# Kernel tuning notes

Measured on AMD Instinct MI355X. Metric: run time of the kernel, lower is better.

The kernel has to match this reference:

```python
import jax, jax.numpy as jnp
import numpy as np

B, S, DIM, FF = 64, 577, 768, 3072
BLK = 8          # block_shape = (8, 8)
DENSITY = 0.1    # fraction of 8x8 blocks that are nonzero


def _expand_block_mask(m):
    # m: [out//BLK, in//BLK] bool -> [out, in] float mask
    return jnp.repeat(jnp.repeat(m, BLK, axis=0), BLK, axis=1)


def setup_inputs() -> dict:
    key = jax.random.key(0)
    ks = jax.random.split(key, 7)
    x = jax.random.normal(ks[0], (B, S, DIM), dtype=jnp.float32)
    # nn.Linear-style init scale
    W1 = jax.random.normal(ks[1], (FF, DIM), dtype=jnp.float32) / np.sqrt(DIM).astype(np.float32)
    b1 = jax.random.normal(ks[2], (FF,), dtype=jnp.float32) * 0.02
    W2 = jax.random.normal(ks[3], (DIM, FF), dtype=jnp.float32) / np.sqrt(FF).astype(np.float32)
    b2 = jax.random.normal(ks[4], (DIM,), dtype=jnp.float32) * 0.02
    mask1 = jax.random.uniform(ks[5], (FF // BLK, DIM // BLK)) < DENSITY
    mask2 = jax.random.uniform(ks[6], (DIM // BLK, FF // BLK)) < DENSITY
    return {"x": x, "W1": W1, "b1": b1, "W2": W2, "b2": b2,
            "mask1": mask1, "mask2": mask2}


def reference(x, W1, b1, W2, b2, mask1, mask2):
    # fc1: block-sparse linear  y = x @ (W1 * M1)^T + b1
    Wm1 = W1 * _expand_block_mask(mask1).astype(W1.dtype)  # [FF, DIM]
    h = jnp.einsum('bsd,fd->bsf', x, Wm1) + b1             # [B, S, FF]
    h = jax.nn.gelu(h, approximate=False)                  # F.gelu default (exact)
    # fc2: block-sparse linear
    Wm2 = W2 * _expand_block_mask(mask2).astype(W2.dtype)  # [DIM, FF]
    return jnp.einsum('bsf,df->bsd', h, Wm2) + b2          # [B, S, DIM]
```

## Files before the change

### kernel.cpp

```cpp
#include <hip/hip_runtime.h>
#include <hip/hip_bf16.h>


typedef __attribute__((ext_vector_type(8))) short short8;
typedef __attribute__((ext_vector_type(4))) float f32x4;
typedef unsigned long long u64;
typedef unsigned short ushort_t;

#define DIM 768
#define FF 3072
#define NF16 192
#define ND16 48
#define NDB 96
#define NFB 384
#define MR 16
#define XP 776
#define HP 1544

#define S1CAP (NF16 * 96)
#define S2CAP (ND16 * 2 * 192)
#define W1S_TOT (S1CAP * 128)
#define W2S_TOT (S2CAP * 128)

__device__ __forceinline__ float gelu_fast(float v) {
    float t = v * fmaf(v * v, 0.07135548f, 1.5957691f);
    return v / (1.0f + __expf(-t));
}
__device__ __forceinline__ ushort_t f2bs(float f) {
    union { __hip_bfloat16 h; ushort_t u; } cv;
    cv.h = __float2bfloat16(f);
    return cv.u;
}

__global__ __launch_bounds__(64)
void prep_count(const int* __restrict__ mask1, const int* __restrict__ mask2,
                int* __restrict__ off1, int* __restrict__ off2)
{
    const int l = threadIdx.x;
    const int g = blockIdx.x;
    if (g < NF16) {
        const int* r0 = mask1 + (2 * g) * NDB;
        const int* r1 = r0 + NDB;
        bool ua = (r0[l] | r1[l]) != 0;
        u64 ba = __ballot(ua);
        bool ub = (l < 32) && ((r0[64 + l] | r1[64 + l]) != 0);
        u64 bb = __ballot(ub);
        if (l == 0) {
            int cnt = __popcll(ba) + __popcll(bb);
            off1[g + 1] = (cnt + 7) & ~7;
        }
    } else {
        const int G = g - NF16;
        const int* r0 = mask2 + (2 * G) * NFB;
        const int* r1 = r0 + NFB;
        int c0 = 0, c1 = 0;
        #pragma unroll
        for (int p = 0; p < 6; ++p) {
            u64 b = __ballot((r0[p * 64 + l] | r1[p * 64 + l]) != 0);
            if (p < 3) c0 += __popcll(b); else c1 += __popcll(b);
        }
        if (l == 0) {
            off2[0 * ND16 + G + 1] = (c0 + 7) & ~7;
            off2[1 * ND16 + G + 1] = (c1 + 7) & ~7;
        }
    }
}

__global__ __launch_bounds__(64)
void prep_scan(int* __restrict__ off1, int* __restrict__ off2)
{
    if (threadIdx.x == 0) {
        off1[0] = 0;
        for (int i = 0; i < NF16; ++i) off1[i + 1] += off1[i];
    } else if (threadIdx.x == 1) {
        off2[0] = 0;
        for (int i = 0; i < 2 * ND16; ++i) off2[i + 1] += off2[i];
    }
}

__global__ __launch_bounds__(256)
void prep_gather(const float* __restrict__ W1, const float* __restrict__ W2,
                 const int* __restrict__ mask1, const int* __restrict__ mask2,
                 const int* __restrict__ off1, const int* __restrict__ off2,
                 __hip_bfloat16* __restrict__ w1s, __hip_bfloat16* __restrict__ w2s,
                 ushort_t* __restrict__ idx1s, ushort_t* __restrict__ idx2s)
{
    __shared__ ushort_t sidx[192];
    __shared__ int sc[1];
    const int tid = threadIdx.x;
    const int l = tid & 63;
    const int g = blockIdx.x;

    if (g < NF16) {
        const int F = g;
        const int* r0 = mask1 + (2 * F) * NDB;
        const int* r1 = r0 + NDB;
        if (tid < 64) {
            bool ua = (r0[l] | r1[l]) != 0;
            u64 ba = __ballot(ua);
            bool ub = (l < 32) && ((r0[64 + l] | r1[64 + l]) != 0);
            u64 bb = __ballot(ub);
            int ca = __popcll(ba);
            if (ua) sidx[__popcll(ba & ((1ull << l) - 1ull))] = (ushort_t)l;
            if (ub) sidx[ca + __popcll(bb & ((1ull << l) - 1ull))] = (ushort_t)(64 + l);
            int cnt = ca + __popcll(bb);
            if (l == 0) {
                sc[0] = cnt;
                int cntp = (cnt + 7) & ~7;
                for (int i = cnt; i < cntp; ++i) sidx[i] = 0;
            }
        }
        __syncthreads();
        const int cnt = sc[0];
        const int base = off1[F];
        const int cntp = off1[F + 1] - base;
        if (tid < cntp) idx1s[base + tid] = sidx[tid];
        for (int e = tid; e < cntp * 128; e += 256) {
            int slot = e >> 7, r = (e >> 3) & 15, j = e & 7;
            int db = sidx[slot];
            float w = 0.f;
            if (slot < cnt && mask1[(2 * F + (r >> 3)) * NDB + db])
                w = W1[(long)(F * 16 + r) * DIM + db * 8 + j];
            w1s[(long)base * 128 + e] = __float2bfloat16(w);
        }
    } else {
        const int gi = g - NF16;
        const int c = gi / ND16;
        const int G = gi % ND16;
        const int* r0 = mask2 + (2 * G) * NFB;
        const int* r1 = r0 + NFB;
        if (tid < 64) {
            u64 b[3]; int pc[3];
            #pragma unroll
            for (int p = 0; p < 3; ++p) {
                int fb = c * 192 + p * 64 + l;
                b[p] = __ballot((r0[fb] | r1[fb]) != 0);
                pc[p] = __popcll(b[p]);
            }
            int basea = 0;
            #pragma unroll
            for (int p = 0; p < 3; ++p) {
                if ((b[p] >> l) & 1ull)
                    sidx[basea + __popcll(b[p] & ((1ull << l) - 1ull))] = (ushort_t)(p * 64 + l);
                basea += pc[p];
            }
            if (l == 0) {
                int cnt = basea;
                sc[0] = cnt;
                int cntp = (cnt + 7) & ~7;
                for (int i = cnt; i < cntp; ++i) sidx[i] = 0;
            }
        }
        __syncthreads();
        const int cnt = sc[0];
        const int base = off2[c * ND16 + G];
        const int cntp = off2[c * ND16 + G + 1] - base;
        if (tid < cntp) idx2s[base + tid] = sidx[tid];
        for (int e = tid; e < cntp * 128; e += 256) {
            int slot = e >> 7, r = (e >> 3) & 15, j = e & 7;
            int lfb = sidx[slot];
            int fb = c * 192 + lfb;
            float w = 0.f;
            if (slot < cnt && mask2[(2 * G + (r >> 3)) * NFB + fb])
                w = W2[(long)(G * 16 + r) * FF + fb * 8 + j];
            w2s[(long)base * 128 + e] = __float2bfloat16(w);
        }
    }
}

#define PREF(IDXS, WS, ARR, ROWOFF)                                          \
    {                                                                        \
        int sp = (s < sEnd) ? s : sEnd - 8;                                  \
        uint4 q = *(const uint4*)(IDXS + sp);                                \
        unsigned dd0 = (lg & 2) ? q.y : q.x;                                 \
        unsigned dd1 = (lg & 2) ? q.w : q.z;                                 \
        int m0 = (int)((dd0 >> shsel) & 0xffffu);                            \
        int m1 = (int)((dd1 >> shsel) & 0xffffu);                            \
        pa0 = *(const short8*)&ARR[ROWOFF + m0 * 8];                         \
        pa1 = *(const short8*)&ARR[ROWOFF + m1 * 8];                         \
        const ushort_t* wp = WS + (long)sp * 128 + lofs;                     \
        pw0 = *(const short8*)(wp);                                          \
        pw1 = *(const short8*)(wp + 512);                                    \
    }

#define STEP(IDXS, WS, ARR, ROWOFF)                                          \
    {                                                                        \
        short8 a0 = pa0, a1 = pa1, w0 = pw0, w1 = pw1;                       \
        s += 8;                                                              \
        PREF(IDXS, WS, ARR, ROWOFF)                                          \
        ca = __builtin_amdgcn_mfma_f32_16x16x32_bf16(a0, w0, ca, 0, 0, 0);   \
        cb = __builtin_amdgcn_mfma_f32_16x16x32_bf16(a1, w1, cb, 0, 0, 0);   \
    }

__global__ __launch_bounds__(512, 4)
void bsffn_main(const float* __restrict__ x,
                const float* __restrict__ pb1, const float* __restrict__ pb2,
                const ushort_t* __restrict__ w1s, const ushort_t* __restrict__ w2s,
                const ushort_t* __restrict__ idx1s, const ushort_t* __restrict__ idx2s,
                const int* __restrict__ off1, const int* __restrict__ off2,
                float* __restrict__ out)
{
    __shared__ __align__(16) ushort_t xs[MR * XP];
    __shared__ __align__(16) ushort_t hs[MR * HP];

    const int tid = threadIdx.x;
    const int wave = tid >> 6;
    const int l = tid & 63;
    const int l15 = l & 15;
    const int lg = l >> 4;
    const int xrow = l15 * XP;
    const int hrow = l15 * HP;
    const int lofs = lg * 128 + l15 * 8;
    const unsigned shsel = (unsigned)((lg & 1) << 4);
    const long rowBase = (long)blockIdx.x * MR;

    {
        const float* xr = x + rowBase * DIM;
        #pragma unroll
        for (int i = 0; i < 3; ++i) {
            int e = tid + i * 512;
            int row = e / 96, c8 = e % 96;
            const float4 v0 = *(const float4*)(xr + row * DIM + c8 * 8);
            const float4 v1 = *(const float4*)(xr + row * DIM + c8 * 8 + 4);
            uint4 wv;
            wv.x = (unsigned)f2bs(v0.x) | ((unsigned)f2bs(v0.y) << 16);
            wv.y = (unsigned)f2bs(v0.z) | ((unsigned)f2bs(v0.w) << 16);
            wv.z = (unsigned)f2bs(v1.x) | ((unsigned)f2bs(v1.y) << 16);
            wv.w = (unsigned)f2bs(v1.z) | ((unsigned)f2bs(v1.w) << 16);
            *(uint4*)&xs[row * XP + c8 * 8] = wv;
        }
    }

    f32x4 acc[6];
    #pragma unroll
    for (int t = 0; t < 6; ++t) acc[t] = (f32x4){0.f, 0.f, 0.f, 0.f};

    __syncthreads();

    for (int chunk = 0; chunk < 2; ++chunk) {
        {
            const int Fbeg = chunk * 96 + wave * 12;
            int s = off1[Fbeg];
            const int sEnd = off1[Fbeg + 12];
            short8 pa0 = {0,0,0,0,0,0,0,0}, pa1 = pa0, pw0 = pa0, pw1 = pa0;
            if (s < sEnd) PREF(idx1s, w1s, xs, xrow)
            #pragma unroll 1
            for (int j = 0; j < 12; ++j) {
                const int F = Fbeg + j;
                const int gend = off1[F + 1];
                const float bias = pb1[F * 16 + l15];
                f32x4 ca = {0.f,0.f,0.f,0.f}, cb = {0.f,0.f,0.f,0.f};
                while (s < gend) STEP(idx1s, w1s, xs, xrow)
                const int Fl = F - chunk * 96;
                #pragma unroll
                for (int r = 0; r < 4; ++r) {
                    float v = gelu_fast(ca[r] + cb[r] + bias);
                    hs[(lg * 4 + r) * HP + Fl * 16 + l15] = f2bs(v);
                }
            }
        }
        __syncthreads();

        {
            const int Pbeg = chunk * ND16 + wave * 6;
            int s = off2[Pbeg];
            const int sEnd = off2[Pbeg + 6];
            short8 pa0 = {0,0,0,0,0,0,0,0}, pa1 = pa0, pw0 = pa0, pw1 = pa0;
            if (s < sEnd) PREF(idx2s, w2s, hs, hrow)
#define FC2G(J)                                                              \
            {                                                                \
                const int gend = off2[Pbeg + (J) + 1];                       \
                f32x4 ca = acc[J], cb = {0.f,0.f,0.f,0.f};                   \
                while (s < gend) STEP(idx2s, w2s, hs, hrow)                  \
                acc[J] = ca + cb;                                            \
            }
            FC2G(0) FC2G(1) FC2G(2) FC2G(3) FC2G(4) FC2G(5)
#undef FC2G
        }
        __syncthreads();
    }

    float* sacc = (float*)hs;
    #pragma unroll
    for (int j = 0; j < 6; ++j) {
        const int d = (wave * 6 + j) * 16 + l15;
        #pragma unroll
        for (int r = 0; r < 4; ++r)
            sacc[(lg * 4 + r) * 772 + d] = acc[j][r];
    }
    __syncthreads();
    {
        const float4* pb24 = (const float4*)pb2;
        #pragma unroll
        for (int i = 0; i < 6; ++i) {
            int e = tid + i * 512;
            int row = e / 192, c4 = e % 192;
            float4 v = *(const float4*)&sacc[row * 772 + c4 * 4];
            float4 b = pb24[c4];
            v.x += b.x; v.y += b.y; v.z += b.z; v.w += b.w;
            *(float4*)&out[(rowBase + row) * DIM + c4 * 4] = v;
        }
    }
}

extern "C" void kernel_launch(void* const* d_in, const int* in_sizes, int n_in,
                              void* d_out, int out_size, void* d_ws, size_t ws_size,
                              hipStream_t stream) {
    const float* x = (const float*)d_in[0];
    const float* W1 = (const float*)d_in[1];
    const float* b1 = (const float*)d_in[2];
    const float* W2 = (const float*)d_in[3];
    const float* b2 = (const float*)d_in[4];
    const int* mask1 = (const int*)d_in[5];
    const int* mask2 = (const int*)d_in[6];
    float* out = (float*)d_out;

    ushort_t* w1s = (ushort_t*)d_ws;
    ushort_t* w2s = w1s + W1S_TOT;
    ushort_t* idx1s = w2s + W2S_TOT;
    ushort_t* idx2s = idx1s + S1CAP;
    int* off1 = (int*)(idx2s + S2CAP);
    int* off2 = off1 + (NF16 + 1);

    prep_count<<<NF16 + ND16, 64, 0, stream>>>(mask1, mask2, off1, off2);
    prep_scan<<<1, 64, 0, stream>>>(off1, off2);
    prep_gather<<<NF16 + 2 * ND16, 256, 0, stream>>>(
        W1, W2, mask1, mask2, off1, off2,
        (__hip_bfloat16*)w1s, (__hip_bfloat16*)w2s, idx1s, idx2s);

    const int rows = in_sizes[0] / DIM;
    const int nblk = rows / MR;
    bsffn_main<<<nblk, 512, 0, stream>>>(
        x, b1, b2, w1s, w2s, idx1s, idx2s, off1, off2, out);
}
```

Measured before the change: 340.7 us.

## Process 32 rows per block to reuse sparse weight fragments across two MFMA row tiles

Doubles the rows per workgroup from 16 to 32 so each loaded sparse weight fragment feeds two MFMA row tiles, halving weight traffic per output row. The slot loop is restructured into double-buffered pair steps of 16 slots, so group padding goes from 8 to 16 and the buffers get extra capacity. GELU is rewritten to use exp2f with prefolded constants. The cost is more registers and shared memory per block, so launch bounds drop to 2 blocks per CU, and the larger padding adds wasted zero MFMAs.

Measured after the change: 335.8 us. About the same (-1.4%).

```diff
diff --git a/kernel.cpp b/kernel.cpp
--- a/kernel.cpp
+++ b/kernel.cpp
@@ -13,18 +13,22 @@
 #define ND16 48
 #define NDB 96
 #define NFB 384
-#define MR 16
+#define MR 32
 #define XP 776
 #define HP 1544
-
-#define S1CAP (NF16 * 96)
-#define S2CAP (ND16 * 2 * 192)
+#define XSEC (16 * XP)
+#define HSEC (16 * HP)
+
+#define S1CAP (NF16 * 96 + 32)
+#define S2CAP (ND16 * 2 * 192 + 32)
 #define W1S_TOT (S1CAP * 128)
 #define W2S_TOT (S2CAP * 128)
 
+#define MFMA __builtin_amdgcn_mfma_f32_16x16x32_bf16
+
 __device__ __forceinline__ float gelu_fast(float v) {
-    float t = v * fmaf(v * v, 0.07135548f, 1.5957691f);
-    return v / (1.0f + __expf(-t));
+    float t2 = v * fmaf(v * v, -0.10295667f, -2.30235629f);
+    return v / (1.0f + exp2f(t2));
 }
 __device__ __forceinline__ ushort_t f2bs(float f) {
     union { __hip_bfloat16 h; ushort_t u; } cv;
@@ -47,7 +51,7 @@
         u64 bb = __ballot(ub);
         if (l == 0) {
             int cnt = __popcll(ba) + __popcll(bb);
-            off1[g + 1] = (cnt + 7) & ~7;
+            off1[g + 1] = (cnt + 15) & ~15;
         }
     } else {
         const int G = g - NF16;
@@ -60,8 +64,8 @@
             if (p < 3) c0 += __popcll(b); else c1 += __popcll(b);
         }
         if (l == 0) {
-            off2[0 * ND16 + G + 1] = (c0 + 7) & ~7;
-            off2[1 * ND16 + G + 1] = (c1 + 7) & ~7;
+            off2[0 * ND16 + G + 1] = (c0 + 15) & ~15;
+            off2[1 * ND16 + G + 1] = (c1 + 15) & ~15;
         }
     }
 }
@@ -106,8 +110,8 @@
             int cnt = ca + __popcll(bb);
             if (l == 0) {
                 sc[0] = cnt;
-                int cntp = (cnt + 7) & ~7;
-                for (int i = cnt; i < cntp; ++i) sidx[i] = 0;
+                int cntp = (cnt + 15) & ~15;
+                for (int i = cnt; i < cntp && i < 192; ++i) sidx[i] = 0;
             }
         }
         __syncthreads();
@@ -147,8 +151,8 @@
             if (l == 0) {
                 int cnt = basea;
                 sc[0] = cnt;
-                int cntp = (cnt + 7) & ~7;
-                for (int i = cnt; i < cntp; ++i) sidx[i] = 0;
+                int cntp = (cnt + 15) & ~15;
+                for (int i = cnt; i < cntp && i < 192; ++i) sidx[i] = 0;
             }
         }
         __syncthreads();
@@ -168,31 +172,37 @@
     }
 }
 
-#define PREF(IDXS, WS, ARR, ROWOFF)                                          \
-    {                                                                        \
-        int sp = (s < sEnd) ? s : sEnd - 8;                                  \
-        uint4 q = *(const uint4*)(IDXS + sp);                                \
-        unsigned dd0 = (lg & 2) ? q.y : q.x;                                 \
-        unsigned dd1 = (lg & 2) ? q.w : q.z;                                 \
-        int m0 = (int)((dd0 >> shsel) & 0xffffu);                            \
-        int m1 = (int)((dd1 >> shsel) & 0xffffu);                            \
-        pa0 = *(const short8*)&ARR[ROWOFF + m0 * 8];                         \
-        pa1 = *(const short8*)&ARR[ROWOFF + m1 * 8];                         \
-        const ushort_t* wp = WS + (long)sp * 128 + lofs;                     \
-        pw0 = *(const short8*)(wp);                                          \
-        pw1 = *(const short8*)(wp + 512);                                    \
-    }
-
-#define STEP(IDXS, WS, ARR, ROWOFF)                                          \
-    {                                                                        \
-        short8 a0 = pa0, a1 = pa1, w0 = pw0, w1 = pw1;                       \
-        s += 8;                                                              \
-        PREF(IDXS, WS, ARR, ROWOFF)                                          \
-        ca = __builtin_amdgcn_mfma_f32_16x16x32_bf16(a0, w0, ca, 0, 0, 0);   \
-        cb = __builtin_amdgcn_mfma_f32_16x16x32_bf16(a1, w1, cb, 0, 0, 0);   \
-    }
-
-__global__ __launch_bounds__(512, 4)
+#define PREF(BUF, IP, WP, ARR, ROWOFF, SECOFF)                          \
+    {                                                                   \
+        uint4 q = *(const uint4*)(IP);                                  \
+        unsigned dd0 = (lg & 2) ? q.y : q.x;                            \
+        unsigned dd1 = (lg & 2) ? q.w : q.z;                            \
+        int mo0 = (int)((dd0 >> shsel) & 0xffffu) * 8;                  \
+        int mo1 = (int)((dd1 >> shsel) & 0xffffu) * 8;                  \
+        BUF##a0 = *(const short8*)&ARR[ROWOFF + mo0];                   \
+        BUF##a1 = *(const short8*)&ARR[ROWOFF + SECOFF + mo0];          \
+        BUF##a2 = *(const short8*)&ARR[ROWOFF + mo1];                   \
+        BUF##a3 = *(const short8*)&ARR[ROWOFF + SECOFF + mo1];          \
+        BUF##w0 = *(const short8*)(WP);                                 \
+        BUF##w1 = *(const short8*)(WP + 512);                           \
+    }
+
+#define PAIRSTEP(IP, WP, ARR, ROWOFF, SECOFF)                           \
+    {                                                                   \
+        short8 t0 = Aa0, t1 = Aa1, t2 = Aa2, t3 = Aa3, u0 = Aw0, u1 = Aw1; \
+        PREF(A, IP, WP, ARR, ROWOFF, SECOFF)                            \
+        ca = MFMA(t0, u0, ca, 0, 0, 0); cc = MFMA(t1, u0, cc, 0, 0, 0); \
+        cb = MFMA(t2, u1, cb, 0, 0, 0); cd = MFMA(t3, u1, cd, 0, 0, 0); \
+    }                                                                   \
+    {                                                                   \
+        short8 t0 = Ba0, t1 = Ba1, t2 = Ba2, t3 = Ba3, u0 = Bw0, u1 = Bw1; \
+        PREF(B, (IP + 8), (WP + 1024), ARR, ROWOFF, SECOFF)             \
+        ca = MFMA(t0, u0, ca, 0, 0, 0); cc = MFMA(t1, u0, cc, 0, 0, 0); \
+        cb = MFMA(t2, u1, cb, 0, 0, 0); cd = MFMA(t3, u1, cd, 0, 0, 0); \
+    }                                                                   \
+    IP += 16; WP += 2048; s += 16;
+
+__global__ __launch_bounds__(512, 2)
 void bsffn_main(const float* __restrict__ x,
                 const float* __restrict__ pb1, const float* __restrict__ pb2,
                 const ushort_t* __restrict__ w1s, const ushort_t* __restrict__ w2s,
@@ -217,7 +227,7 @@
     {
         const float* xr = x + rowBase * DIM;
         #pragma unroll
-        for (int i = 0; i < 3; ++i) {
+        for (int i = 0; i < 6; ++i) {
             int e = tid + i * 512;
             int row = e / 96, c8 = e % 96;
             const float4 v0 = *(const float4*)(xr + row * DIM + c8 * 8);
@@ -231,9 +241,12 @@
         }
     }
 
-    f32x4 acc[6];
+    f32x4 acc0[6], acc1[6];
     #pragma unroll
-    for (int t = 0; t < 6; ++t) acc[t] = (f32x4){0.f, 0.f, 0.f, 0.f};
+    for (int t = 0; t < 6; ++t) {
+        acc0[t] = (f32x4){0.f, 0.f, 0.f, 0.f};
+        acc1[t] = (f32x4){0.f, 0.f, 0.f, 0.f};
+    }
 
     __syncthreads();
 
@@ -241,21 +254,24 @@
         {
             const int Fbeg = chunk * 96 + wave * 12;
             int s = off1[Fbeg];
-            const int sEnd = off1[Fbeg + 12];
-            short8 pa0 = {0,0,0,0,0,0,0,0}, pa1 = pa0, pw0 = pa0, pw1 = pa0;
-            if (s < sEnd) PREF(idx1s, w1s, xs, xrow)
+            const ushort_t* ip = idx1s + s;
+            const ushort_t* wp = w1s + (long)s * 128 + lofs;
+            short8 Aa0, Aa1, Aa2, Aa3, Aw0, Aw1, Ba0, Ba1, Ba2, Ba3, Bw0, Bw1;
+            PREF(A, ip, wp, xs, xrow, XSEC)
+            PREF(B, (ip + 8), (wp + 1024), xs, xrow, XSEC)
+            ip += 16; wp += 2048;
             #pragma unroll 1
             for (int j = 0; j < 12; ++j) {
                 const int F = Fbeg + j;
                 const int gend = off1[F + 1];
+                f32x4 ca = {0.f,0.f,0.f,0.f}, cb = ca, cc = ca, cd = ca;
+                while (s < gend) { PAIRSTEP(ip, wp, xs, xrow, XSEC) }
                 const float bias = pb1[F * 16 + l15];
-                f32x4 ca = {0.f,0.f,0.f,0.f}, cb = {0.f,0.f,0.f,0.f};
-                while (s < gend) STEP(idx1s, w1s, xs, xrow)
-                const int Fl = F - chunk * 96;
+                const int hcol = (F - chunk * 96) * 16 + l15;
                 #pragma unroll
                 for (int r = 0; r < 4; ++r) {
-                    float v = gelu_fast(ca[r] + cb[r] + bias);
-                    hs[(lg * 4 + r) * HP + Fl * 16 + l15] = f2bs(v);
+                    hs[(lg * 4 + r) * HP + hcol] = f2bs(gelu_fast(ca[r] + cb[r] + bias));
+                    hs[HSEC + (lg * 4 + r) * HP + hcol] = f2bs(gelu_fast(cc[r] + cd[r] + bias));
                 }
             }
         }
@@ -264,15 +280,19 @@
         {
             const int Pbeg = chunk * ND16 + wave * 6;
             int s = off2[Pbeg];
-            const int sEnd = off2[Pbeg + 6];
-            short8 pa0 = {0,0,0,0,0,0,0,0}, pa1 = pa0, pw0 = pa0, pw1 = pa0;
-            if (s < sEnd) PREF(idx2s, w2s, hs, hrow)
-#define FC2G(J)                                                              \
-            {                                                                \
-                const int gend = off2[Pbeg + (J) + 1];                       \
-                f32x4 ca = acc[J], cb = {0.f,0.f,0.f,0.f};                   \
-                while (s < gend) STEP(idx2s, w2s, hs, hrow)                  \
-                acc[J] = ca + cb;                                            \
+            const ushort_t* ip = idx2s + s;
+            const ushort_t* wp = w2s + (long)s * 128 + lofs;
+            short8 Aa0, Aa1, Aa2, Aa3, Aw0, Aw1, Ba0, Ba1, Ba2, Ba3, Bw0, Bw1;
+            PREF(A, ip, wp, hs, hrow, HSEC)
+            PREF(B, (ip + 8), (wp + 1024), hs, hrow, HSEC)
+            ip += 16; wp += 2048;
+#define FC2G(J)                                                          \
+            {                                                            \
+                const int gend = off2[Pbeg + (J) + 1];                   \
+                f32x4 ca = acc0[J], cc = acc1[J];                        \
+                f32x4 cb = {0.f,0.f,0.f,0.f}, cd = cb;                   \
+                while (s < gend) { PAIRSTEP(ip, wp, hs, hrow, HSEC) }    \
+                acc0[J] = ca + cb; acc1[J] = cc + cd;                    \
             }
             FC2G(0) FC2G(1) FC2G(2) FC2G(3) FC2G(4) FC2G(5)
 #undef FC2G
@@ -285,14 +305,16 @@
     for (int j = 0; j < 6; ++j) {
         const int d = (wave * 6 + j) * 16 + l15;
         #pragma unroll
-        for (int r = 0; r < 4; ++r)
-            sacc[(lg * 4 + r) * 772 + d] = acc[j][r];
+        for (int r = 0; r < 4; ++r) {
+            sacc[(lg * 4 + r) * 772 + d] = acc0[j][r];
+            sacc[(16 + lg * 4 + r) * 772 + d] = acc1[j][r];
+        }
     }
     __syncthreads();
     {
         const float4* pb24 = (const float4*)pb2;
         #pragma unroll
-        for (int i = 0; i < 6; ++i) {
+        for (int i = 0; i < 12; ++i) {
             int e = tid + i * 512;
             int row = e / 192, c4 = e % 192;
             float4 v = *(const float4*)&sacc[row * 772 + c4 * 4];
```
